# Performance work log

Measured on AMD Instinct MI355X. Metric: run time of the kernel, lower is better.

The kernel has to match this reference:

```python
import jax, jax.numpy as jnp
import numpy as np

H = 512
W = 512


def setup_inputs() -> dict:
    key = jax.random.key(0)
    k1, k2 = jax.random.split(key)
    B, P, C = 8, 30000, 64
    pillar_features = jax.random.normal(k1, (B, P, C), dtype=jnp.float32)
    pillar_coords = jax.random.randint(k2, (B, P, 2), 0, 512, dtype=jnp.int32)
    return {"pillar_features": pillar_features, "pillar_coords": pillar_coords}


def _scatter_one(feat, coords):
    # feat: (P, C), coords: (P, 2) as [gx, gy]
    gx = coords[:, 0]
    gy = coords[:, 1]
    valid = (gx >= 0) & (gx < W) & (gy >= 0) & (gy < H)
    # invalid pillars -> out-of-range flat index, dropped by mode='drop'
    flat = jnp.where(valid, gy * W + gx, H * W)
    bev = jnp.zeros((H * W, feat.shape[1]), dtype=feat.dtype)
    bev = bev.at[flat].set(feat, mode="drop")
    # (H*W, C) -> (C, H, W)
    return bev.reshape(H, W, -1).transpose(2, 0, 1)


def reference(pillar_features, pillar_coords):
    return jax.vmap(_scatter_one)(pillar_features, pillar_coords)
```

## Files before the change

### kernel.cpp

```cpp
#include <hip/hip_runtime.h>

#define BEV_H 512
#define BEV_W 512
#define BEV_HW (BEV_H * BEV_W)
#define NB 8
#define NP 30000
#define NC 64

__global__ void scatter_winner_kernel(const int* __restrict__ coords,
                                      int* __restrict__ winner) {
    int idx = blockIdx.x * blockDim.x + threadIdx.x;
    if (idx >= NB * NP) return;
    int b = idx / NP;
    int p = idx - b * NP;
    int2 c2 = ((const int2*)coords)[idx];
    int gx = c2.x;
    int gy = c2.y;
    if (gx >= 0 && gx < BEV_W && gy >= 0 && gy < BEV_H) {
        atomicMax(&winner[b * BEV_HW + gy * BEV_W + gx], p);
    }
}

__global__ void gather_out_kernel(const float* __restrict__ feat,
                                  const int* __restrict__ winner,
                                  float* __restrict__ out) {
    int b = blockIdx.y;
    int cell = blockIdx.x * blockDim.x + threadIdx.x;

    int w = winner[b * BEV_HW + cell];

    float4 r[16];
    if (w >= 0) {
        const float4* row = (const float4*)(feat + ((size_t)b * NP + w) * NC);
        #pragma unroll
        for (int j = 0; j < 16; ++j) r[j] = row[j];
    } else {
        #pragma unroll
        for (int j = 0; j < 16; ++j) r[j] = make_float4(0.f, 0.f, 0.f, 0.f);
    }

    float* o = out + (size_t)b * NC * BEV_HW + cell;
    #pragma unroll
    for (int j = 0; j < 16; ++j) {
        o[(size_t)(4 * j + 0) * BEV_HW] = r[j].x;
        o[(size_t)(4 * j + 1) * BEV_HW] = r[j].y;
        o[(size_t)(4 * j + 2) * BEV_HW] = r[j].z;
        o[(size_t)(4 * j + 3) * BEV_HW] = r[j].w;
    }
}

extern "C" void kernel_launch(void* const* d_in, const int* in_sizes, int n_in,
                              void* d_out, int out_size, void* d_ws, size_t ws_size,
                              hipStream_t stream) {
    const float* feat   = (const float*)d_in[0];
    const int*   coords = (const int*)d_in[1];
    float*       out    = (float*)d_out;
    int*         winner = (int*)d_ws;

    hipMemsetAsync(winner, 0xFF, (size_t)NB * BEV_HW * sizeof(int), stream);

    {
        int total = NB * NP;
        int block = 256;
        int grid  = (total + block - 1) / block;
        scatter_winner_kernel<<<grid, block, 0, stream>>>(coords, winner);
    }

    {
        dim3 block(256, 1, 1);
        dim3 grid(BEV_HW / 256, NB, 1);
        gather_out_kernel<<<grid, block, 0, stream>>>(feat, winner, out);
    }
}
```

Measured before the change: 609.2 us.

## Vectorize gather stores: each thread handles 4 cells × 16 channels with float4 writes

```diff
diff --git a/kernel.cpp b/kernel.cpp
--- a/kernel.cpp
+++ b/kernel.cpp
@@ -21,31 +21,41 @@
     }
 }
 
-__global__ void gather_out_kernel(const float* __restrict__ feat,
-                                  const int* __restrict__ winner,
-                                  float* __restrict__ out) {
-    int b = blockIdx.y;
-    int cell = blockIdx.x * blockDim.x + threadIdx.x;
+__global__ void __launch_bounds__(256)
+gather_out_kernel(const float* __restrict__ feat,
+                  const int* __restrict__ winner,
+                  float* __restrict__ out) {
+    int b  = blockIdx.y;
+    int t  = threadIdx.x;
+    int cg = t & 63;
+    int cq = t >> 6;
+    int cell0 = blockIdx.x * 256 + 4 * cg;
 
-    int w = winner[b * BEV_HW + cell];
+    const int4 w4 = *(const int4*)(winner + b * BEV_HW + cell0);
+    const int w[4] = {w4.x, w4.y, w4.z, w4.w};
 
-    float4 r[16];
-    if (w >= 0) {
-        const float4* row = (const float4*)(feat + ((size_t)b * NP + w) * NC);
-        #pragma unroll
-        for (int j = 0; j < 16; ++j) r[j] = row[j];
-    } else {
-        #pragma unroll
-        for (int j = 0; j < 16; ++j) r[j] = make_float4(0.f, 0.f, 0.f, 0.f);
+    const float* fb = feat + (size_t)b * NP * NC + 16 * cq;
+
+    float q[4][16];
+    #pragma unroll
+    for (int j = 0; j < 4; ++j) {
+        if (w[j] >= 0) {
+            const float4* row = (const float4*)(fb + (size_t)w[j] * NC);
+            *(float4*)&q[j][0]  = row[0];
+            *(float4*)&q[j][4]  = row[1];
+            *(float4*)&q[j][8]  = row[2];
+            *(float4*)&q[j][12] = row[3];
+        } else {
+            #pragma unroll
+            for (int i = 0; i < 16; ++i) q[j][i] = 0.0f;
+        }
     }
 
-    float* o = out + (size_t)b * NC * BEV_HW + cell;
+    float* o = out + ((size_t)b * NC + 16 * cq) * BEV_HW + cell0;
     #pragma unroll
-    for (int j = 0; j < 16; ++j) {
-        o[(size_t)(4 * j + 0) * BEV_HW] = r[j].x;
-        o[(size_t)(4 * j + 1) * BEV_HW] = r[j].y;
-        o[(size_t)(4 * j + 2) * BEV_HW] = r[j].z;
-        o[(size_t)(4 * j + 3) * BEV_HW] = r[j].w;
+    for (int i = 0; i < 16; ++i) {
+        float4 v = make_float4(q[0][i], q[1][i], q[2][i], q[3][i]);
+        *(float4*)(o + (size_t)i * BEV_HW) = v;
     }
 }
 
```

After: 596.5 us. 1.02x faster.
